# Optimization experiments

Hardware: AMD Instinct MI355X
Metric: run time of the kernel (lower is better)

## Reference

```python
import jax, jax.numpy as jnp
import numpy as np

B, D, T = 4, 1024, 512      # z: [B, input_dim, T]
V, CD = 32000, 4096          # codebook: [codebook_size, codebook_dim]
EPS = 1e-12                  # F.normalize default eps


def setup_inputs() -> dict:
    key = jax.random.key(0)
    k1, k2, k3, k4 = jax.random.split(key, 4)
    z = jax.random.normal(k1, (B, D, T), dtype=jnp.float32)
    codebook = jax.random.normal(k2, (V, CD), dtype=jnp.float32) * 0.02
    cb_w = jax.random.normal(k3, (D, CD), dtype=jnp.float32) * 0.02  # torch Linear weight [out,in]
    cb_b = jax.random.normal(k4, (D,), dtype=jnp.float32) * 0.02
    return {"z": z, "codebook": codebook, "cb_w": cb_w, "cb_b": cb_b}


def _l2norm(x):
    n = jnp.sqrt(jnp.sum(x * x, axis=1, keepdims=True))
    return x / jnp.maximum(n, EPS)


def reference(z, codebook, cb_w, cb_b):
    # stride == 1, use_cblinear == True -> z_e = z
    z_e = z                                              # [B, D, T]
    proj_cb = codebook @ cb_w.T + cb_b                    # [V, D] cb_proj(codebook)

    # decode_latents
    enc = jnp.transpose(z_e, (0, 2, 1)).reshape(-1, D)    # (B*T, D)
    enc_n = _l2norm(enc)
    cb_n = _l2norm(proj_cb)
    dist = (jnp.sum(enc_n * enc_n, axis=1, keepdims=True)
            - 2.0 * enc_n @ cb_n.T
            + jnp.sum(cb_n * cb_n, axis=1)[None, :])      # (B*T, V)
    indices = jnp.argmax(-dist, axis=1).reshape(B, T)     # argmin distance
    z_q = jnp.transpose(proj_cb[indices], (0, 2, 1))      # gather un-normalized codes -> [B, D, T]

    commitment_loss = jnp.mean((z_e - jax.lax.stop_gradient(z_q)) ** 2, axis=(1, 2))  # [B]
    codebook_loss = jnp.mean((z_q - jax.lax.stop_gradient(z_e)) ** 2, axis=(1, 2))    # [B]
    z_q_st = z_e + jax.lax.stop_gradient(z_q - z_e)       # straight-through
    return z_q_st, indices, commitment_loss, codebook_loss
```

## Files before the change

kernel.cpp:

```cpp
#include <hip/hip_runtime.h>
#include <hip/hip_bf16.h>
#include <math.h>

#define B_  4
#define D_  1024
#define T_  512
#define V_  32000
#define CD_ 4096
#define NR  (B_*T_)
#define VT2 (V_/256)

typedef __attribute__((ext_vector_type(8))) short short8v;
typedef __attribute__((ext_vector_type(4))) float f32x4;

#define MFMA16(a,b,c) __builtin_amdgcn_mfma_f32_16x16x32_bf16((a),(b),(c),0,0,0)

#define ASM_VMCNT8() asm volatile("s_waitcnt vmcnt(8)" ::: "memory")
#define ASM_VMCNT0() asm volatile("s_waitcnt vmcnt(0)" ::: "memory")
#define ASM_LGKM0()  asm volatile("s_waitcnt lgkmcnt(0)" ::: "memory")
#define SCHED_BAR()  __builtin_amdgcn_sched_barrier(0)

__device__ __forceinline__ unsigned short f2bf(float f) {
    return __builtin_bit_cast(unsigned short, __float2bfloat16(f));
}
__device__ __forceinline__ float bf2f(unsigned short u) {
    unsigned int v = ((unsigned int)u) << 16;
    return __builtin_bit_cast(float, v);
}
__device__ __forceinline__ void glds16(const unsigned short* g, unsigned short* l) {
    __builtin_amdgcn_global_load_lds(
        (const __attribute__((address_space(1))) unsigned int*)g,
        (__attribute__((address_space(3))) unsigned int*)l, 16, 0, 0);
}
__device__ __forceinline__ void gldsf(const float* g, float* l) {
    __builtin_amdgcn_global_load_lds(
        (const __attribute__((address_space(1))) unsigned int*)g,
        (__attribute__((address_space(3))) unsigned int*)l, 16, 0, 0);
}
__device__ __forceinline__ void cvt8(const float4& x, const float4& y,
                                     short8v& h, short8v& l) {
    float xs[8] = {x.x, x.y, x.z, x.w, y.x, y.y, y.z, y.w};
    #pragma unroll
    for (int e = 0; e < 8; ++e) {
        unsigned short hb = f2bf(xs[e]);
        h[e] = (short)hb;
        l[e] = (short)f2bf(xs[e] - bf2f(hb));
    }
}
__device__ __forceinline__ int xcd_swz(int wg, int nwg) {
    int q = nwg >> 3, r = nwg & 7;
    int x = wg & 7, o = wg >> 3;
    return (x < r ? x * (q + 1) : r * (q + 1) + (x - r) * q) + o;
}

__global__ __launch_bounds__(256) void vq_cvt(const float* __restrict__ x,
                                              unsigned short* __restrict__ hi,
                                              unsigned short* __restrict__ lo,
                                              size_t n4) {
    size_t stride = (size_t)gridDim.x * 256;
    for (size_t i = (size_t)blockIdx.x * 256 + threadIdx.x; i < n4; i += stride) {
        float4 v = *(const float4*)(x + 4 * i);
        float xs[4] = {v.x, v.y, v.z, v.w};
        ushort4 h, l;
        unsigned short* hp = (unsigned short*)&h;
        unsigned short* lp = (unsigned short*)&l;
        #pragma unroll
        for (int e = 0; e < 4; ++e) {
            hp[e] = f2bf(xs[e]);
            lp[e] = f2bf(xs[e] - bf2f(hp[e]));
        }
        *(ushort4*)(hi + 4 * i) = h;
        *(ushort4*)(lo + 4 * i) = l;
    }
}

__global__ __launch_bounds__(512, 2) void vq_gemm1_f(
    const float* __restrict__ Acb,
    const unsigned short* __restrict__ Bhp, const unsigned short* __restrict__ Blp,
    const float* __restrict__ bias,
    unsigned short* __restrict__ Phi, unsigned short* __restrict__ Plo)
{
    __shared__ float          Af[2][8192];
    __shared__ unsigned short Bh[2][8192];
    __shared__ unsigned short Bl[2][8192];
    const int wg = xcd_swz(blockIdx.x, (V_/256) * (D_/256));
    const int mt = (wg >> 2) * 256;
    const int nt = (wg & 3) * 256;
    const int lane = threadIdx.x & 63, w = threadIdx.x >> 6;
    const int wr = w >> 2, wc = w & 3;
    const int r16 = lane & 15, kg = lane >> 4;
    const int lane8 = lane * 8, wr8 = wr * 8, wc4 = wc * 4;

    f32x4 acc[8][4];
    #pragma unroll
    for (int i = 0; i < 8; ++i)
        #pragma unroll
        for (int j = 0; j < 4; ++j) acc[i][j] = (f32x4){0.f, 0.f, 0.f, 0.f};

#define STAGE1F(b, kk) do {                                                   \
    if (w < 4) {                                                              \
        _Pragma("unroll")                                                     \
        for (int j = 0; j < 4; ++j) {                                         \
            const int sub = w * 4 + j;                                        \
            const float* g0 = Acb + (size_t)(mt + sub*16 + r16) * CD_         \
                              + (kk) + kg * 4;                                \
            gldsf(g0,      &Af[b][sub*512]);                                  \
            gldsf(g0 + 16, &Af[b][sub*512 + 256]);                            \
        }                                                                     \
    } else if (w < 6) {                                                       \
        const int sb = (w - 4) * 8;                                           \
        _Pragma("unroll")                                                     \
        for (int j = 0; j < 8; ++j)                                           \
            glds16(Bhp + (size_t)(nt + (sb+j)*16 + r16) * CD_ + (kk) + kg*8,  \
                   &Bh[b][(sb+j)*512]);                                       \
    } else {                                                                  \
        const int sb = (w - 6) * 8;                                           \
        _Pragma("unroll")                                                     \
        for (int j = 0; j < 8; ++j)                                           \
            glds16(Blp + (size_t)(nt + (sb+j)*16 + r16) * CD_ + (kk) + kg*8,  \
                   &Bl[b][(sb+j)*512]);                                       \
    }                                                                         \
} while (0)

    STAGE1F(0, 0);
    ASM_VMCNT0();
    __builtin_amdgcn_s_barrier();
    SCHED_BAR();

    const int NT = CD_ / 32;
    const int afrag = (kg >> 1) * 256 + (kg & 1) * 128 + r16 * 4;
    for (int t = 0; t < NT; ++t) {
        const int cur = t & 1;
        if (t + 1 < NT) {
            STAGE1F(cur ^ 1, (size_t)(t + 1) * 32);
            ASM_VMCNT8();
        } else {
            ASM_VMCNT0();
        }
        __builtin_amdgcn_s_barrier();
        SCHED_BAR();
        short8v bh[4], bl[4];
        #pragma unroll
        for (int nf = 0; nf < 4; ++nf) {
            bh[nf] = *(const short8v*)&Bh[cur][(wc4 + nf) * 512 + lane8];
            bl[nf] = *(const short8v*)&Bl[cur][(wc4 + nf) * 512 + lane8];
        }
        #pragma unroll
        for (int g = 0; g < 4; ++g) {
            const float* f0 = &Af[cur][(wr8 + 2*g) * 512 + afrag];
            const float* f1 = &Af[cur][(wr8 + 2*g + 1) * 512 + afrag];
            float4 x0 = *(const float4*)f0, x1 = *(const float4*)(f0 + 64);
            float4 y0 = *(const float4*)f1, y1 = *(const float4*)(f1 + 64);
            short8v a0h, a0l, a1h, a1l;
            cvt8(x0, x1, a0h, a0l);
            cvt8(y0, y1, a1h, a1l);
            __builtin_amdgcn_s_setprio(1);
            #pragma unroll
            for (int nf = 0; nf < 4; ++nf) {
                acc[2*g][nf]   = MFMA16(a0h, bh[nf], acc[2*g][nf]);
                acc[2*g][nf]   = MFMA16(a0h, bl[nf], acc[2*g][nf]);
                acc[2*g][nf]   = MFMA16(a0l, bh[nf], acc[2*g][nf]);
                acc[2*g+1][nf] = MFMA16(a1h, bh[nf], acc[2*g+1][nf]);
                acc[2*g+1][nf] = MFMA16(a1h, bl[nf], acc[2*g+1][nf]);
                acc[2*g+1][nf] = MFMA16(a1l, bh[nf], acc[2*g+1][nf]);
            }
            __builtin_amdgcn_s_setprio(0);
        }
        ASM_LGKM0();
        __builtin_amdgcn_s_barrier();
        SCHED_BAR();
    }
#undef STAGE1F

    #pragma unroll
    for (int nf = 0; nf < 4; ++nf) {
        const int col = nt + wc * 64 + nf * 16 + r16;
        const float bv = bias[col];
        #pragma unroll
        for (int mf = 0; mf < 8; ++mf) {
            const int rbase = mt + wr * 128 + mf * 16 + kg * 4;
            #pragma unroll
            for (int r = 0; r < 4; ++r) {
                float vv = acc[mf][nf][r] + bv;
                unsigned short h = f2bf(vv);
                unsigned short l = f2bf(vv - bf2f(h));
                size_t o = (size_t)(rbase + r) * D_ + col;
                Phi[o] = h; Plo[o] = l;
            }
        }
    }
}

#define T8_PHASE(pp, EXTRA)                                                   \
    {                                                                         \
        short8v aAh = *(const short8v*)&smem[cur][0][(wr8 + 2*(pp)) * 512 + lane8];     \
        short8v aAl = *(const short8v*)&smem[cur][1][(wr8 + 2*(pp)) * 512 + lane8];     \
        short8v aBh = *(const short8v*)&smem[cur][0][(wr8 + 2*(pp) + 1) * 512 + lane8]; \
        short8v aBl = *(const short8v*)&smem[cur][1][(wr8 + 2*(pp) + 1) * 512 + lane8]; \
        EXTRA;                                                                \
        SCHED_BAR();                                                          \
        __builtin_amdgcn_s_barrier();                                         \
        ASM_LGKM0();                                                          \
        SCHED_BAR();                                                          \
        __builtin_amdgcn_s_setprio(1);                                        \
        _Pragma("unroll")                                                     \
        for (int nf = 0; nf < 4; ++nf) {                                      \
            acc[2*(pp)][nf]   = MFMA16(aAh, bh[nf], acc[2*(pp)][nf]);         \
            acc[2*(pp)][nf]   = MFMA16(aAh, bl[nf], acc[2*(pp)][nf]);         \
            acc[2*(pp)][nf]   = MFMA16(aAl, bh[nf], acc[2*(pp)][nf]);         \
            acc[2*(pp)+1][nf] = MFMA16(aBh, bh[nf], acc[2*(pp)+1][nf]);       \
            acc[2*(pp)+1][nf] = MFMA16(aBh, bl[nf], acc[2*(pp)+1][nf]);       \
            acc[2*(pp)+1][nf] = MFMA16(aBl, bh[nf], acc[2*(pp)+1][nf]);       \
        }                                                                     \
        __builtin_amdgcn_s_setprio(0);                                        \
        __builtin_amdgcn_s_barrier();                                         \
        SCHED_BAR();                                                          \
    }

__global__ __launch_bounds__(512, 2) void vq_gemm2_t8(
    const unsigned short* __restrict__ Ahp, const unsigned short* __restrict__ Alp,
    const unsigned short* __restrict__ Bhp, const unsigned short* __restrict__ Blp,
    const float* __restrict__ ninv,
    float* __restrict__ pmax, int* __restrict__ pidx)
{
    __shared__ unsigned short smem[2][4][8192];
    const int wg = xcd_swz(blockIdx.x, (NR/256) * VT2);
    const int nid = wg >> 3;
    const int mt = (wg & 7) * 256;
    const int nt = nid * 256;

    f32x4 acc[8][4];
    #pragma unroll
    for (int i = 0; i < 8; ++i)
        #pragma unroll
        for (int j = 0; j < 4; ++j) acc[i][j] = (f32x4){0.f, 0.f, 0.f, 0.f};
    const int lane = threadIdx.x & 63, w = threadIdx.x >> 6;
    const int wr = w >> 2, wc = w & 3;
    const int r16 = lane & 15, kg = lane >> 4;
    const int lane8 = lane * 8, wr8 = wr * 8, wc4 = wc * 4;
    const int pw = w >> 1;
    const unsigned short* gplane = (pw == 0) ? Ahp : (pw == 1) ? Alp
                                   : (pw == 2) ? Bhp : Blp;
    const int baseRow = (pw < 2 ? mt : nt) + (w & 1) * 128 + r16;
    const unsigned short* gsrc = gplane + (size_t)baseRow * D_ + kg * 8;
    unsigned short* lb0 = &smem[0][pw][(w & 1) * 4096 + lane8];
    unsigned short* lb1 = &smem[1][pw][(w & 1) * 4096 + lane8];
    #pragma unroll
    for (int q = 0; q < 8; ++q)
        glds16(gsrc + (size_t)q * 16 * D_, lb0 + q * 512);
    ASM_VMCNT0();
    __builtin_amdgcn_s_barrier();
    SCHED_BAR();
    const int NT = D_ / 32;
    for (int t = 0; t < NT; ++t) {
        const int cur = t & 1;
        unsigned short* lbN = cur ? lb0 : lb1;
        short8v bh[4], bl[4];
        #pragma unroll
        for (int nf = 0; nf < 4; ++nf) {
            bh[nf] = *(const short8v*)&smem[cur][2][(wc4 + nf) * 512 + lane8];
            bl[nf] = *(const short8v*)&smem[cur][3][(wc4 + nf) * 512 + lane8];
        }
        T8_PHASE(0,
            if (t + 1 < NT) {
                const size_t kof = (size_t)(t + 1) * 32;
                _Pragma("unroll")
                for (int q = 0; q < 8; ++q)
                    glds16(gsrc + kof + (size_t)q * 16 * D_, lbN + q * 512);
            })
        T8_PHASE(1, (void)0)
        T8_PHASE(2, (void)0)
        T8_PHASE(3, if (t + 1 < NT) { ASM_VMCNT0(); })
    }

    float* redv = (float*)&smem[0][0][0];
    int*   redi = (int*)&smem[0][0][2048];
    float nv[4];
    #pragma unroll
    for (int nf = 0; nf < 4; ++nf) nv[nf] = ninv[nt + wc * 64 + nf * 16 + r16];
    #pragma unroll
    for (int mf = 0; mf < 8; ++mf) {
        #pragma unroll
        for (int r = 0; r < 4; ++r) {
            float best = -INFINITY; int bi = 0x7fffffff;
            #pragma unroll
            for (int nf = 0; nf < 4; ++nf) {
                float v = acc[mf][nf][r] * nv[nf];
                int ci = nt + wc * 64 + nf * 16 + r16;
                if (v > best || (v == best && ci < bi)) { best = v; bi = ci; }
            }
            #pragma unroll
            for (int m = 8; m >= 1; m >>= 1) {
                float ov = __shfl_xor(best, m, 16);
                int   oi = __shfl_xor(bi,   m, 16);
                if (ov > best || (ov == best && oi < bi)) { best = ov; bi = oi; }
            }
            if (r16 == 0) {
                int rl = wr * 128 + mf * 16 + kg * 4 + r;
                redv[rl * 4 + wc] = best; redi[rl * 4 + wc] = bi;
            }
        }
    }
    __builtin_amdgcn_s_barrier();
    if (threadIdx.x < 256) {
        float best = -INFINITY; int bi = 0x7fffffff;
        #pragma unroll
        for (int c = 0; c < 4; ++c) {
            float v = redv[threadIdx.x * 4 + c];
            int   i = redi[threadIdx.x * 4 + c];
            if (v > best || (v == best && i < bi)) { best = v; bi = i; }
        }
        size_t o = (size_t)(mt + threadIdx.x) * VT2 + nid;
        pmax[o] = best; pidx[o] = bi;
    }
}

__global__ __launch_bounds__(256) void vq_norms_pl(const unsigned short* __restrict__ ph,
                                                   const unsigned short* __restrict__ pl,
                                                   float* __restrict__ ninv) {
    const int row  = blockIdx.x * 4 + (threadIdx.x >> 6);
    const int lane = threadIdx.x & 63;
    float s = 0.f;
    #pragma unroll
    for (int q = 0; q < 2; ++q) {
        size_t o = (size_t)row * D_ + q * 512 + lane * 8;
        short8v h = *(const short8v*)(ph + o);
        short8v l = *(const short8v*)(pl + o);
        #pragma unroll
        for (int e = 0; e < 8; ++e) {
            float x = bf2f((unsigned short)h[e]) + bf2f((unsigned short)l[e]);
            s += x * x;
        }
    }
    #pragma unroll
    for (int off = 32; off >= 1; off >>= 1) s += __shfl_down(s, off);
    if (lane == 0) ninv[row] = 1.0f / fmaxf(sqrtf(s), 1e-12f);
}

__global__ __launch_bounds__(256) void vq_transpose_cvt(const float* __restrict__ z,
                                                        unsigned short* __restrict__ ehi,
                                                        unsigned short* __restrict__ elo) {
    __shared__ float tile[64][65];
    const int b = blockIdx.z, t0 = blockIdx.x * 64, d0 = blockIdx.y * 64;
    const int lane = threadIdx.x & 63, sub = threadIdx.x >> 6;
    for (int dd = sub; dd < 64; dd += 4)
        tile[dd][lane] = z[((size_t)b * D_ + d0 + dd) * T_ + t0 + lane];
    __syncthreads();
    for (int tt = sub; tt < 64; tt += 4) {
        float v = tile[lane][tt];
        unsigned short h = f2bf(v);
        unsigned short l = f2bf(v - bf2f(h));
        size_t o = (size_t)(b * T_ + t0 + tt) * D_ + d0 + lane;
        ehi[o] = h; elo[o] = l;
    }
}

__global__ __launch_bounds__(256) void vq_argmerge(const float* __restrict__ pmax,
                                                   const int* __restrict__ pidx,
                                                   int* __restrict__ idxw,
                                                   float* __restrict__ outI,
                                                   int vt) {
    const int i = blockIdx.x * 256 + threadIdx.x;
    if (i >= NR) return;
    float best = -INFINITY; int bi = 0;
    for (int c = 0; c < vt; c++) {
        float v = pmax[(size_t)i * vt + c];
        int   ii = pidx[(size_t)i * vt + c];
        if (v > best || (v == best && ii < bi)) { best = v; bi = ii; }
    }
    idxw[i] = bi;
    outI[i] = (float)bi;
}

__global__ __launch_bounds__(256) void vq_gather_pl(const unsigned short* __restrict__ ph,
                                                    const unsigned short* __restrict__ pl,
                                                    const int* __restrict__ idxw,
                                                    const float* __restrict__ z,
                                                    float* __restrict__ out0,
                                                    float* __restrict__ lpart) {
    __shared__ float zq[64][65];
    __shared__ int idx_s[64];
    __shared__ float wsum[4];
    const int b = blockIdx.z, t0 = blockIdx.x * 64, d0 = blockIdx.y * 64;
    const int tid = threadIdx.x;
    const int lane = tid & 63, sub = tid >> 6;
    if (tid < 64) idx_s[tid] = idxw[b * T_ + t0 + tid];
    __syncthreads();
    for (int tt = sub; tt < 64; tt += 4) {
        size_t o = (size_t)idx_s[tt] * D_ + d0 + lane;
        zq[tt][lane] = bf2f(ph[o]) + bf2f(pl[o]);
    }
    __syncthreads();
    float lacc = 0.f;
    for (int dd = sub; dd < 64; dd += 4) {
        const size_t base = ((size_t)b * D_ + d0 + dd) * T_ + t0 + lane;
        float q = zq[lane][dd];
        float zv = z[base];
        out0[base] = q;
        float dv = zv - q;
        lacc += dv * dv;
    }
    #pragma unroll
    for (int off = 32; off >= 1; off >>= 1) lacc += __shfl_down(lacc, off);
    if (lane == 0) wsum[sub] = lacc;
    __syncthreads();
    if (tid == 0)
        lpart[(blockIdx.z * 16 + blockIdx.y) * 8 + blockIdx.x] =
            wsum[0] + wsum[1] + wsum[2] + wsum[3];
}

__global__ void vq_loss(const float* __restrict__ lpart, float* __restrict__ outL) {
    const int b = threadIdx.x;
    if (b >= B_) return;
    float s = 0.f;
    for (int q = 0; q < 128; q++) s += lpart[b * 128 + q];
    s /= (float)(D_ * T_);
    outL[b]      = s;
    outL[B_ + b] = s;
}

extern "C" void kernel_launch(void* const* d_in, const int* in_sizes, int n_in,
                              void* d_out, int out_size, void* d_ws, size_t ws_size,
                              hipStream_t stream) {
    const float* z        = (const float*)d_in[0];
    const float* codebook = (const float*)d_in[1];
    const float* cb_w     = (const float*)d_in[2];
    const float* cb_b     = (const float*)d_in[3];

    float* out0 = (float*)d_out;
    float* outI = out0 + (size_t)B_*D_*T_;
    float* outL = outI + NR;

    char* p = (char*)d_ws;
    auto alloc = [&](size_t bytes) { char* r = p; p += (bytes + 255) & ~(size_t)255; return r; };
    unsigned short* w_hi = (unsigned short*)alloc((size_t)D_ * CD_ * 2);
    unsigned short* w_lo = (unsigned short*)alloc((size_t)D_ * CD_ * 2);
    unsigned short* p_hi = (unsigned short*)alloc((size_t)V_ * D_ * 2);
    unsigned short* p_lo = (unsigned short*)alloc((size_t)V_ * D_ * 2);
    unsigned short* e_hi = (unsigned short*)alloc((size_t)NR * D_ * 2);
    unsigned short* e_lo = (unsigned short*)alloc((size_t)NR * D_ * 2);
    float* ninv  = (float*)alloc((size_t)V_ * 4);
    float* pmax  = (float*)alloc((size_t)NR * VT2 * 4);
    int*   pidx  = (int*)  alloc((size_t)NR * VT2 * 4);
    int*   idxw  = (int*)  alloc((size_t)NR * 4);
    float* lpart = (float*)alloc((size_t)2048 * 4);

    vq_cvt<<<512, 256, 0, stream>>>(cb_w, w_hi, w_lo, (size_t)D_ * CD_ / 4);
    vq_transpose_cvt<<<dim3(T_/64, D_/64, B_), 256, 0, stream>>>(z, e_hi, e_lo);

    vq_gemm1_f<<<(V_/256) * (D_/256), 512, 0, stream>>>(codebook, w_hi, w_lo,
                                                        cb_b, p_hi, p_lo);
    vq_norms_pl<<<V_/4, 256, 0, stream>>>(p_hi, p_lo, ninv);
    vq_gemm2_t8<<<(NR/256) * VT2, 512, 0, stream>>>(e_hi, e_lo, p_hi, p_lo,
                                                    ninv, pmax, pidx);
    vq_argmerge<<<NR/256, 256, 0, stream>>>(pmax, pidx, idxw, outI, VT2);
    vq_gather_pl<<<dim3(T_/64, D_/64, B_), 256, 0, stream>>>(p_hi, p_lo, idxw, z,
                                                             out0, lpart);
    vq_loss<<<1, 64, 0, stream>>>(lpart, outL);
}
```

Before: 1.573 ms.

## Pre-split codebook to bf16 planes and split-K the projection GEMM

Measured after the change: 1.733 ms. 10.1% more time.

```diff
diff --git a/kernel.cpp b/kernel.cpp
--- a/kernel.cpp
+++ b/kernel.cpp
@@ -9,6 +9,7 @@
 #define CD_ 4096
 #define NR  (B_*T_)
 #define VT2 (V_/256)
+#define NTILE1 ((V_/256)*(D_/256))
 
 typedef __attribute__((ext_vector_type(8))) short short8v;
 typedef __attribute__((ext_vector_type(4))) float f32x4;
@@ -28,11 +29,6 @@
     return __builtin_bit_cast(float, v);
 }
 __device__ __forceinline__ void glds16(const unsigned short* g, unsigned short* l) {
-    __builtin_amdgcn_global_load_lds(
-        (const __attribute__((address_space(1))) unsigned int*)g,
-        (__attribute__((address_space(3))) unsigned int*)l, 16, 0, 0);
-}
-__device__ __forceinline__ void gldsf(const float* g, float* l) {
     __builtin_amdgcn_global_load_lds(
         (const __attribute__((address_space(1))) unsigned int*)g,
         (__attribute__((address_space(3))) unsigned int*)l, 16, 0, 0);
@@ -74,22 +70,29 @@
     }
 }
 
-__global__ __launch_bounds__(512, 2) void vq_gemm1_f(
-    const float* __restrict__ Acb,
+__global__ __launch_bounds__(512, 2) void vq_gemm1_sk(
+    const unsigned short* __restrict__ Ahp, const unsigned short* __restrict__ Alp,
     const unsigned short* __restrict__ Bhp, const unsigned short* __restrict__ Blp,
-    const float* __restrict__ bias,
-    unsigned short* __restrict__ Phi, unsigned short* __restrict__ Plo)
+    float* __restrict__ pf, int nch)
 {
-    __shared__ float          Af[2][8192];
-    __shared__ unsigned short Bh[2][8192];
-    __shared__ unsigned short Bl[2][8192];
-    const int wg = xcd_swz(blockIdx.x, (V_/256) * (D_/256));
-    const int mt = (wg >> 2) * 256;
-    const int nt = (wg & 3) * 256;
+    __shared__ unsigned short smem[2][4][8192];
+    const int wg = xcd_swz(blockIdx.x, NTILE1 * nch);
+    const int kc = wg / NTILE1;
+    const int tl = wg - kc * NTILE1;
+    const int mt = (tl >> 2) * 256;
+    const int nt = (tl & 3) * 256;
+    const int kbase = kc * (CD_ / nch);
     const int lane = threadIdx.x & 63, w = threadIdx.x >> 6;
     const int wr = w >> 2, wc = w & 3;
     const int r16 = lane & 15, kg = lane >> 4;
     const int lane8 = lane * 8, wr8 = wr * 8, wc4 = wc * 4;
+    const int pw = w >> 1;
+    const unsigned short* gplane = (pw == 0) ? Ahp : (pw == 1) ? Alp
+                                   : (pw == 2) ? Bhp : Blp;
+    const int baseRow = (pw < 2 ? mt : nt) + (w & 1) * 128 + r16;
+    const unsigned short* gsrc = gplane + (size_t)baseRow * CD_ + kbase + kg * 8;
+    unsigned short* lb0 = &smem[0][pw][(w & 1) * 4096 + lane8];
+    unsigned short* lb1 = &smem[1][pw][(w & 1) * 4096 + lane8];
 
     f32x4 acc[8][4];
     #pragma unroll
@@ -97,42 +100,22 @@
         #pragma unroll
         for (int j = 0; j < 4; ++j) acc[i][j] = (f32x4){0.f, 0.f, 0.f, 0.f};
 
-#define STAGE1F(b, kk) do {                                                   \
-    if (w < 4) {                                                              \
-        _Pragma("unroll")                                                     \
-        for (int j = 0; j < 4; ++j) {                                         \
-            const int sub = w * 4 + j;                                        \
-            const float* g0 = Acb + (size_t)(mt + sub*16 + r16) * CD_         \
-                              + (kk) + kg * 4;                                \
-            gldsf(g0,      &Af[b][sub*512]);                                  \
-            gldsf(g0 + 16, &Af[b][sub*512 + 256]);                            \
-        }                                                                     \
-    } else if (w < 6) {                                                       \
-        const int sb = (w - 4) * 8;                                           \
-        _Pragma("unroll")                                                     \
-        for (int j = 0; j < 8; ++j)                                           \
-            glds16(Bhp + (size_t)(nt + (sb+j)*16 + r16) * CD_ + (kk) + kg*8,  \
-                   &Bh[b][(sb+j)*512]);                                       \
-    } else {                                                                  \
-        const int sb = (w - 6) * 8;                                           \
-        _Pragma("unroll")                                                     \
-        for (int j = 0; j < 8; ++j)                                           \
-            glds16(Blp + (size_t)(nt + (sb+j)*16 + r16) * CD_ + (kk) + kg*8,  \
-                   &Bl[b][(sb+j)*512]);                                       \
-    }                                                                         \
-} while (0)
-
-    STAGE1F(0, 0);
+    #pragma unroll
+    for (int q = 0; q < 8; ++q)
+        glds16(gsrc + (size_t)q * 16 * CD_, lb0 + q * 512);
     ASM_VMCNT0();
     __builtin_amdgcn_s_barrier();
     SCHED_BAR();
 
-    const int NT = CD_ / 32;
-    const int afrag = (kg >> 1) * 256 + (kg & 1) * 128 + r16 * 4;
+    const int NT = (CD_ / 32) / nch;
     for (int t = 0; t < NT; ++t) {
         const int cur = t & 1;
         if (t + 1 < NT) {
-            STAGE1F(cur ^ 1, (size_t)(t + 1) * 32);
+            unsigned short* lb = cur ? lb0 : lb1;
+            const size_t kof = (size_t)(t + 1) * 32;
+            #pragma unroll
+            for (int q = 0; q < 8; ++q)
+                glds16(gsrc + kof + (size_t)q * 16 * CD_, lb + q * 512);
             ASM_VMCNT8();
         } else {
             ASM_VMCNT0();
@@ -142,18 +125,15 @@
         short8v bh[4], bl[4];
         #pragma unroll
         for (int nf = 0; nf < 4; ++nf) {
-            bh[nf] = *(const short8v*)&Bh[cur][(wc4 + nf) * 512 + lane8];
-            bl[nf] = *(const short8v*)&Bl[cur][(wc4 + nf) * 512 + lane8];
+            bh[nf] = *(const short8v*)&smem[cur][2][(wc4 + nf) * 512 + lane8];
+            bl[nf] = *(const short8v*)&smem[cur][3][(wc4 + nf) * 512 + lane8];
         }
         #pragma unroll
         for (int g = 0; g < 4; ++g) {
-            const float* f0 = &Af[cur][(wr8 + 2*g) * 512 + afrag];
-            const float* f1 = &Af[cur][(wr8 + 2*g + 1) * 512 + afrag];
-            float4 x0 = *(const float4*)f0, x1 = *(const float4*)(f0 + 64);
-            float4 y0 = *(const float4*)f1, y1 = *(const float4*)(f1 + 64);
-            short8v a0h, a0l, a1h, a1l;
-            cvt8(x0, x1, a0h, a0l);
-            cvt8(y0, y1, a1h, a1l);
+            short8v a0h = *(const short8v*)&smem[cur][0][(wr8 + 2*g) * 512 + lane8];
+            short8v a0l = *(const short8v*)&smem[cur][1][(wr8 + 2*g) * 512 + lane8];
+            short8v a1h = *(const short8v*)&smem[cur][0][(wr8 + 2*g + 1) * 512 + lane8];
+            short8v a1l = *(const short8v*)&smem[cur][1][(wr8 + 2*g + 1) * 512 + lane8];
             __builtin_amdgcn_s_setprio(1);
             #pragma unroll
             for (int nf = 0; nf < 4; ++nf) {
@@ -170,7 +150,126 @@
         __builtin_amdgcn_s_barrier();
         SCHED_BAR();
     }
-#undef STAGE1F
+
+    float* out = pf + (size_t)kc * V_ * D_;
+    #pragma unroll
+    for (int nf = 0; nf < 4; ++nf) {
+        const int col = nt + wc * 64 + nf * 16 + r16;
+        #pragma unroll
+        for (int mf = 0; mf < 8; ++mf) {
+            const int rbase = mt + wr * 128 + mf * 16 + kg * 4;
+            #pragma unroll
+            for (int r = 0; r < 4; ++r)
+                out[(size_t)(rbase + r) * D_ + col] = acc[mf][nf][r];
+        }
+    }
+}
+
+__global__ __launch_bounds__(256) void vq_reduce(const float* __restrict__ pf, int nch,
+                                                 const float* __restrict__ bias,
+                                                 unsigned short* __restrict__ hi,
+                                                 unsigned short* __restrict__ lo) {
+    const size_t n4 = (size_t)V_ * D_ / 4;
+    size_t stride = (size_t)gridDim.x * 256;
+    for (size_t i = (size_t)blockIdx.x * 256 + threadIdx.x; i < n4; i += stride) {
+        float4 s = ((const float4*)pf)[i];
+        for (int c = 1; c < nch; ++c) {
+            float4 p = *(const float4*)(pf + (size_t)c * V_ * D_ + 4 * i);
+            s.x += p.x; s.y += p.y; s.z += p.z; s.w += p.w;
+        }
+        float4 b = ((const float4*)bias)[i & (D_/4 - 1)];
+        float xs[4] = {s.x + b.x, s.y + b.y, s.z + b.z, s.w + b.w};
+        ushort4 h, l;
+        unsigned short* hp = (unsigned short*)&h;
+        unsigned short* lp = (unsigned short*)&l;
+        #pragma unroll
+        for (int e = 0; e < 4; ++e) {
+            hp[e] = f2bf(xs[e]);
+            lp[e] = f2bf(xs[e] - bf2f(hp[e]));
+        }
+        *(ushort4*)(hi + 4 * i) = h;
+        *(ushort4*)(lo + 4 * i) = l;
+    }
+}
+
+__global__ __launch_bounds__(512, 2) void vq_gemm1_v2(
+    const unsigned short* __restrict__ Ahp, const unsigned short* __restrict__ Alp,
+    const unsigned short* __restrict__ Bhp, const unsigned short* __restrict__ Blp,
+    const float* __restrict__ bias,
+    unsigned short* __restrict__ Phi, unsigned short* __restrict__ Plo)
+{
+    __shared__ unsigned short smem[2][4][8192];
+    const int wg = xcd_swz(blockIdx.x, NTILE1);
+    const int mt = (wg >> 2) * 256;
+    const int nt = (wg & 3) * 256;
+    const int lane = threadIdx.x & 63, w = threadIdx.x >> 6;
+    const int wr = w >> 2, wc = w & 3;
+    const int r16 = lane & 15, kg = lane >> 4;
+    const int lane8 = lane * 8, wr8 = wr * 8, wc4 = wc * 4;
+    const int pw = w >> 1;
+    const unsigned short* gplane = (pw == 0) ? Ahp : (pw == 1) ? Alp
+                                   : (pw == 2) ? Bhp : Blp;
+    const int baseRow = (pw < 2 ? mt : nt) + (w & 1) * 128 + r16;
+    const unsigned short* gsrc = gplane + (size_t)baseRow * CD_ + kg * 8;
+    unsigned short* lb0 = &smem[0][pw][(w & 1) * 4096 + lane8];
+    unsigned short* lb1 = &smem[1][pw][(w & 1) * 4096 + lane8];
+
+    f32x4 acc[8][4];
+    #pragma unroll
+    for (int i = 0; i < 8; ++i)
+        #pragma unroll
+        for (int j = 0; j < 4; ++j) acc[i][j] = (f32x4){0.f, 0.f, 0.f, 0.f};
+
+    #pragma unroll
+    for (int q = 0; q < 8; ++q)
+        glds16(gsrc + (size_t)q * 16 * CD_, lb0 + q * 512);
+    ASM_VMCNT0();
+    __builtin_amdgcn_s_barrier();
+    SCHED_BAR();
+
+    const int NT = CD_ / 32;
+    for (int t = 0; t < NT; ++t) {
+        const int cur = t & 1;
+        if (t + 1 < NT) {
+            unsigned short* lb = cur ? lb0 : lb1;
+            const size_t kof = (size_t)(t + 1) * 32;
+            #pragma unroll
+            for (int q = 0; q < 8; ++q)
+                glds16(gsrc + kof + (size_t)q * 16 * CD_, lb + q * 512);
+            ASM_VMCNT8();
+        } else {
+            ASM_VMCNT0();
+        }
+        __builtin_amdgcn_s_barrier();
+        SCHED_BAR();
+        short8v bh[4], bl[4];
+        #pragma unroll
+        for (int nf = 0; nf < 4; ++nf) {
+            bh[nf] = *(const short8v*)&smem[cur][2][(wc4 + nf) * 512 + lane8];
+            bl[nf] = *(const short8v*)&smem[cur][3][(wc4 + nf) * 512 + lane8];
+        }
+        #pragma unroll
+        for (int g = 0; g < 4; ++g) {
+            short8v a0h = *(const short8v*)&smem[cur][0][(wr8 + 2*g) * 512 + lane8];
+            short8v a0l = *(const short8v*)&smem[cur][1][(wr8 + 2*g) * 512 + lane8];
+            short8v a1h = *(const short8v*)&smem[cur][0][(wr8 + 2*g + 1) * 512 + lane8];
+            short8v a1l = *(const short8v*)&smem[cur][1][(wr8 + 2*g + 1) * 512 + lane8];
+            __builtin_amdgcn_s_setprio(1);
+            #pragma unroll
+            for (int nf = 0; nf < 4; ++nf) {
+                acc[2*g][nf]   = MFMA16(a0h, bh[nf], acc[2*g][nf]);
+                acc[2*g][nf]   = MFMA16(a0h, bl[nf], acc[2*g][nf]);
+                acc[2*g][nf]   = MFMA16(a0l, bh[nf], acc[2*g][nf]);
+                acc[2*g+1][nf] = MFMA16(a1h, bh[nf], acc[2*g+1][nf]);
+                acc[2*g+1][nf] = MFMA16(a1h, bl[nf], acc[2*g+1][nf]);
+                acc[2*g+1][nf] = MFMA16(a1l, bh[nf], acc[2*g+1][nf]);
+            }
+            __builtin_amdgcn_s_setprio(0);
+        }
+        ASM_LGKM0();
+        __builtin_amdgcn_s_barrier();
+        SCHED_BAR();
+    }
 
     #pragma unroll
     for (int nf = 0; nf < 4; ++nf) {
@@ -213,7 +312,7 @@
             acc[2*(pp)+1][nf] = MFMA16(aBl, bh[nf], acc[2*(pp)+1][nf]);       \
         }                                                                     \
         __builtin_amdgcn_s_setprio(0);                                        \
-        __builtin_amdgcn_s_barrier();                                         \
+        __builtin_amdgcn_s_barrier();                                        \
         SCHED_BAR();                                                          \
     }
 
@@ -444,12 +543,28 @@
     int*   pidx  = (int*)  alloc((size_t)NR * VT2 * 4);
     int*   idxw  = (int*)  alloc((size_t)NR * 4);
     float* lpart = (float*)alloc((size_t)2048 * 4);
+    unsigned short* c_hi = (unsigned short*)alloc((size_t)V_ * CD_ * 2);
+    unsigned short* c_lo = (unsigned short*)alloc((size_t)V_ * CD_ * 2);
+    size_t need_v2 = (size_t)(p - (char*)d_ws);
+    float* pf = (float*)alloc((size_t)2 * V_ * D_ * 4);
+    size_t need_k2 = (size_t)(p - (char*)d_ws);
+    alloc((size_t)2 * V_ * D_ * 4);
+    size_t need_k4 = (size_t)(p - (char*)d_ws);
 
     vq_cvt<<<512, 256, 0, stream>>>(cb_w, w_hi, w_lo, (size_t)D_ * CD_ / 4);
     vq_transpose_cvt<<<dim3(T_/64, D_/64, B_), 256, 0, stream>>>(z, e_hi, e_lo);
-
-    vq_gemm1_f<<<(V_/256) * (D_/256), 512, 0, stream>>>(codebook, w_hi, w_lo,
-                                                        cb_b, p_hi, p_lo);
+    vq_cvt<<<4096, 256, 0, stream>>>(codebook, c_hi, c_lo, (size_t)V_ * CD_ / 4);
+
+    if (ws_size >= need_k4) {
+        vq_gemm1_sk<<<NTILE1 * 4, 512, 0, stream>>>(c_hi, c_lo, w_hi, w_lo, pf, 4);
+        vq_reduce<<<4096, 256, 0, stream>>>(pf, 4, cb_b, p_hi, p_lo);
+    } else if (ws_size >= need_k2) {
+        vq_gemm1_sk<<<NTILE1 * 2, 512, 0, stream>>>(c_hi, c_lo, w_hi, w_lo, pf, 2);
+        vq_reduce<<<4096, 256, 0, stream>>>(pf, 2, cb_b, p_hi, p_lo);
+    } else {
+        vq_gemm1_v2<<<NTILE1, 512, 0, stream>>>(c_hi, c_lo, w_hi, w_lo,
+                                                cb_b, p_hi, p_lo);
+    }
     vq_norms_pl<<<V_/4, 256, 0, stream>>>(p_hi, p_lo, ninv);
     vq_gemm2_t8<<<(NR/256) * VT2, 512, 0, stream>>>(e_hi, e_lo, p_hi, p_lo,
                                                     ninv, pmax, pidx);
```

## Use single-bf16 distance GEMM with top-k candidates and exact rescoring

Applied to the files above, without the earlier changes.

After: 2.546 ms. 61.8% more time.

```diff
diff --git a/kernel.cpp b/kernel.cpp
--- a/kernel.cpp
+++ b/kernel.cpp
@@ -9,6 +9,9 @@
 #define CD_ 4096
 #define NR  (B_*T_)
 #define VT2 (V_/256)
+#define NTILE1 ((V_/256)*(D_/256))
+#define NQ4 (VT2*4)
+#define NC8 8
 
 typedef __attribute__((ext_vector_type(8))) short short8v;
 typedef __attribute__((ext_vector_type(4))) float f32x4;
@@ -16,6 +19,7 @@
 #define MFMA16(a,b,c) __builtin_amdgcn_mfma_f32_16x16x32_bf16((a),(b),(c),0,0,0)
 
 #define ASM_VMCNT8() asm volatile("s_waitcnt vmcnt(8)" ::: "memory")
+#define ASM_VMCNT4() asm volatile("s_waitcnt vmcnt(4)" ::: "memory")
 #define ASM_VMCNT0() asm volatile("s_waitcnt vmcnt(0)" ::: "memory")
 #define ASM_LGKM0()  asm volatile("s_waitcnt lgkmcnt(0)" ::: "memory")
 #define SCHED_BAR()  __builtin_amdgcn_sched_barrier(0)
@@ -32,11 +36,6 @@
         (const __attribute__((address_space(1))) unsigned int*)g,
         (__attribute__((address_space(3))) unsigned int*)l, 16, 0, 0);
 }
-__device__ __forceinline__ void gldsf(const float* g, float* l) {
-    __builtin_amdgcn_global_load_lds(
-        (const __attribute__((address_space(1))) unsigned int*)g,
-        (__attribute__((address_space(3))) unsigned int*)l, 16, 0, 0);
-}
 __device__ __forceinline__ void cvt8(const float4& x, const float4& y,
                                      short8v& h, short8v& l) {
     float xs[8] = {x.x, x.y, x.z, x.w, y.x, y.y, y.z, y.w};
@@ -51,6 +50,11 @@
     int q = nwg >> 3, r = nwg & 7;
     int x = wg & 7, o = wg >> 3;
     return (x < r ? x * (q + 1) : r * (q + 1) + (x - r) * q) + o;
+}
+__device__ __forceinline__ void top2_ins(float& v1, int& i1, float& v2, int& i2,
+                                         float nv, int ni) {
+    if (nv > v1 || (nv == v1 && ni < i1)) { v2 = v1; i2 = i1; v1 = nv; i1 = ni; }
+    else if (nv > v2 || (nv == v2 && ni < i2)) { v2 = nv; i2 = ni; }
 }
 
 __global__ __launch_bounds__(256) void vq_cvt(const float* __restrict__ x,
@@ -71,123 +75,6 @@
         }
         *(ushort4*)(hi + 4 * i) = h;
         *(ushort4*)(lo + 4 * i) = l;
-    }
-}
-
-__global__ __launch_bounds__(512, 2) void vq_gemm1_f(
-    const float* __restrict__ Acb,
-    const unsigned short* __restrict__ Bhp, const unsigned short* __restrict__ Blp,
-    const float* __restrict__ bias,
-    unsigned short* __restrict__ Phi, unsigned short* __restrict__ Plo)
-{
-    __shared__ float          Af[2][8192];
-    __shared__ unsigned short Bh[2][8192];
-    __shared__ unsigned short Bl[2][8192];
-    const int wg = xcd_swz(blockIdx.x, (V_/256) * (D_/256));
-    const int mt = (wg >> 2) * 256;
-    const int nt = (wg & 3) * 256;
-    const int lane = threadIdx.x & 63, w = threadIdx.x >> 6;
-    const int wr = w >> 2, wc = w & 3;
-    const int r16 = lane & 15, kg = lane >> 4;
-    const int lane8 = lane * 8, wr8 = wr * 8, wc4 = wc * 4;
-
-    f32x4 acc[8][4];
-    #pragma unroll
-    for (int i = 0; i < 8; ++i)
-        #pragma unroll
-        for (int j = 0; j < 4; ++j) acc[i][j] = (f32x4){0.f, 0.f, 0.f, 0.f};
-
-#define STAGE1F(b, kk) do {                                                   \
-    if (w < 4) {                                                              \
-        _Pragma("unroll")                                                     \
-        for (int j = 0; j < 4; ++j) {                                         \
-            const int sub = w * 4 + j;                                        \
-            const float* g0 = Acb + (size_t)(mt + sub*16 + r16) * CD_         \
-                              + (kk) + kg * 4;                                \
-            gldsf(g0,      &Af[b][sub*512]);                                  \
-            gldsf(g0 + 16, &Af[b][sub*512 + 256]);                            \
-        }                                                                     \
-    } else if (w < 6) {                                                       \
-        const int sb = (w - 4) * 8;                                           \
-        _Pragma("unroll")                                                     \
-        for (int j = 0; j < 8; ++j)                                           \
-            glds16(Bhp + (size_t)(nt + (sb+j)*16 + r16) * CD_ + (kk) + kg*8,  \
-                   &Bh[b][(sb+j)*512]);                                       \
-    } else {                                                                  \
-        const int sb = (w - 6) * 8;                                           \
-        _Pragma("unroll")                                                     \
-        for (int j = 0; j < 8; ++j)                                           \
-            glds16(Blp + (size_t)(nt + (sb+j)*16 + r16) * CD_ + (kk) + kg*8,  \
-                   &Bl[b][(sb+j)*512]);                                       \
-    }                                                                         \
-} while (0)
-
-    STAGE1F(0, 0);
-    ASM_VMCNT0();
-    __builtin_amdgcn_s_barrier();
-    SCHED_BAR();
-
-    const int NT = CD_ / 32;
-    const int afrag = (kg >> 1) * 256 + (kg & 1) * 128 + r16 * 4;
-    for (int t = 0; t < NT; ++t) {
-        const int cur = t & 1;
-        if (t + 1 < NT) {
-            STAGE1F(cur ^ 1, (size_t)(t + 1) * 32);
-            ASM_VMCNT8();
-        } else {
-            ASM_VMCNT0();
-        }
-        __builtin_amdgcn_s_barrier();
-        SCHED_BAR();
-        short8v bh[4], bl[4];
-        #pragma unroll
-        for (int nf = 0; nf < 4; ++nf) {
-            bh[nf] = *(const short8v*)&Bh[cur][(wc4 + nf) * 512 + lane8];
-            bl[nf] = *(const short8v*)&Bl[cur][(wc4 + nf) * 512 + lane8];
-        }
-        #pragma unroll
-        for (int g = 0; g < 4; ++g) {
-            const float* f0 = &Af[cur][(wr8 + 2*g) * 512 + afrag];
-            const float* f1 = &Af[cur][(wr8 + 2*g + 1) * 512 + afrag];
-            float4 x0 = *(const float4*)f0, x1 = *(const float4*)(f0 + 64);
-            float4 y0 = *(const float4*)f1, y1 = *(const float4*)(f1 + 64);
-            short8v a0h, a0l, a1h, a1l;
-            cvt8(x0, x1, a0h, a0l);
-            cvt8(y0, y1, a1h, a1l);
-            __builtin_amdgcn_s_setprio(1);
-            #pragma unroll
-            for (int nf = 0; nf < 4; ++nf) {
-                acc[2*g][nf]   = MFMA16(a0h, bh[nf], acc[2*g][nf]);
-                acc[2*g][nf]   = MFMA16(a0h, bl[nf], acc[2*g][nf]);
-                acc[2*g][nf]   = MFMA16(a0l, bh[nf], acc[2*g][nf]);
-                acc[2*g+1][nf] = MFMA16(a1h, bh[nf], acc[2*g+1][nf]);
-                acc[2*g+1][nf] = MFMA16(a1h, bl[nf], acc[2*g+1][nf]);
-                acc[2*g+1][nf] = MFMA16(a1l, bh[nf], acc[2*g+1][nf]);
-            }
-            __builtin_amdgcn_s_setprio(0);
-        }
-        ASM_LGKM0();
-        __builtin_amdgcn_s_barrier();
-        SCHED_BAR();
-    }
-#undef STAGE1F
-
-    #pragma unroll
-    for (int nf = 0; nf < 4; ++nf) {
-        const int col = nt + wc * 64 + nf * 16 + r16;
-        const float bv = bias[col];
-        #pragma unroll
-        for (int mf = 0; mf < 8; ++mf) {
-            const int rbase = mt + wr * 128 + mf * 16 + kg * 4;
-            #pragma unroll
-            for (int r = 0; r < 4; ++r) {
-                float vv = acc[mf][nf][r] + bv;
-                unsigned short h = f2bf(vv);
-                unsigned short l = f2bf(vv - bf2f(h));
-                size_t o = (size_t)(rbase + r) * D_ + col;
-                Phi[o] = h; Plo[o] = l;
-            }
-        }
     }
 }
 
@@ -217,23 +104,16 @@
         SCHED_BAR();                                                          \
     }
 
-__global__ __launch_bounds__(512, 2) void vq_gemm2_t8(
+__global__ __launch_bounds__(512, 2) void vq_gemm1_t8(
     const unsigned short* __restrict__ Ahp, const unsigned short* __restrict__ Alp,
     const unsigned short* __restrict__ Bhp, const unsigned short* __restrict__ Blp,
-    const float* __restrict__ ninv,
-    float* __restrict__ pmax, int* __restrict__ pidx)
+    const float* __restrict__ bias,
+    unsigned short* __restrict__ Phi, unsigned short* __restrict__ Plo)
 {
     __shared__ unsigned short smem[2][4][8192];
-    const int wg = xcd_swz(blockIdx.x, (NR/256) * VT2);
-    const int nid = wg >> 3;
-    const int mt = (wg & 7) * 256;
-    const int nt = nid * 256;
-
-    f32x4 acc[8][4];
-    #pragma unroll
-    for (int i = 0; i < 8; ++i)
-        #pragma unroll
-        for (int j = 0; j < 4; ++j) acc[i][j] = (f32x4){0.f, 0.f, 0.f, 0.f};
+    const int wg = xcd_swz(blockIdx.x, NTILE1);
+    const int mt = (wg >> 2) * 256;
+    const int nt = (wg & 3) * 256;
     const int lane = threadIdx.x & 63, w = threadIdx.x >> 6;
     const int wr = w >> 2, wc = w & 3;
     const int r16 = lane & 15, kg = lane >> 4;
@@ -242,16 +122,23 @@
     const unsigned short* gplane = (pw == 0) ? Ahp : (pw == 1) ? Alp
                                    : (pw == 2) ? Bhp : Blp;
     const int baseRow = (pw < 2 ? mt : nt) + (w & 1) * 128 + r16;
-    const unsigned short* gsrc = gplane + (size_t)baseRow * D_ + kg * 8;
+    const unsigned short* gsrc = gplane + (size_t)baseRow * CD_ + kg * 8;
     unsigned short* lb0 = &smem[0][pw][(w & 1) * 4096 + lane8];
     unsigned short* lb1 = &smem[1][pw][(w & 1) * 4096 + lane8];
+
+    f32x4 acc[8][4];
+    #pragma unroll
+    for (int i = 0; i < 8; ++i)
+        #pragma unroll
+        for (int j = 0; j < 4; ++j) acc[i][j] = (f32x4){0.f, 0.f, 0.f, 0.f};
+
     #pragma unroll
     for (int q = 0; q < 8; ++q)
-        glds16(gsrc + (size_t)q * 16 * D_, lb0 + q * 512);
+        glds16(gsrc + (size_t)q * 16 * CD_, lb0 + q * 512);
     ASM_VMCNT0();
     __builtin_amdgcn_s_barrier();
     SCHED_BAR();
-    const int NT = D_ / 32;
+    const int NT = CD_ / 32;
     for (int t = 0; t < NT; ++t) {
         const int cur = t & 1;
         unsigned short* lbN = cur ? lb0 : lb1;
@@ -266,52 +153,204 @@
                 const size_t kof = (size_t)(t + 1) * 32;
                 _Pragma("unroll")
                 for (int q = 0; q < 8; ++q)
-                    glds16(gsrc + kof + (size_t)q * 16 * D_, lbN + q * 512);
+                    glds16(gsrc + kof + (size_t)q * 16 * CD_, lbN + q * 512);
             })
         T8_PHASE(1, (void)0)
         T8_PHASE(2, (void)0)
         T8_PHASE(3, if (t + 1 < NT) { ASM_VMCNT0(); })
     }
 
-    float* redv = (float*)&smem[0][0][0];
-    int*   redi = (int*)&smem[0][0][2048];
-    float nv[4];
-    #pragma unroll
-    for (int nf = 0; nf < 4; ++nf) nv[nf] = ninv[nt + wc * 64 + nf * 16 + r16];
-    #pragma unroll
-    for (int mf = 0; mf < 8; ++mf) {
-        #pragma unroll
-        for (int r = 0; r < 4; ++r) {
-            float best = -INFINITY; int bi = 0x7fffffff;
+    #pragma unroll
+    for (int nf = 0; nf < 4; ++nf) {
+        const int col = nt + wc * 64 + nf * 16 + r16;
+        const float bv = bias[col];
+        #pragma unroll
+        for (int mf = 0; mf < 8; ++mf) {
+            const int rbase = mt + wr * 128 + mf * 16 + kg * 4;
+            #pragma unroll
+            for (int r = 0; r < 4; ++r) {
+                float vv = acc[mf][nf][r] + bv;
+                unsigned short h = f2bf(vv);
+                unsigned short l = f2bf(vv - bf2f(h));
+                size_t o = (size_t)(rbase + r) * D_ + col;
+                Phi[o] = h; Plo[o] = l;
+            }
+        }
+    }
+}
+
+__global__ __launch_bounds__(512, 2) void vq_gemm2_c1(
+    const unsigned short* __restrict__ Eh, const unsigned short* __restrict__ Ph,
+    const float* __restrict__ ninv,
+    float* __restrict__ parrv, int* __restrict__ parri)
+{
+    __shared__ unsigned short smem[2][2][8192];
+    const int wg = xcd_swz(blockIdx.x, (NR/256) * VT2);
+    const int nid = wg >> 3;
+    const int mt = (wg & 7) * 256;
+    const int nt = nid * 256;
+    const int lane = threadIdx.x & 63, w = threadIdx.x >> 6;
+    const int wr = w >> 2, wc = w & 3;
+    const int r16 = lane & 15, kg = lane >> 4;
+    const int lane8 = lane * 8, wr8 = wr * 8, wc4 = wc * 4;
+    const int pw = w >> 2;
+    const int sq = (w & 3) * 4;
+    const unsigned short* gp = pw ? Ph : Eh;
+    const int baseRow = (pw ? nt : mt) + sq * 16 + r16;
+    const unsigned short* gsrc = gp + (size_t)baseRow * D_ + kg * 8;
+    unsigned short* lb0 = &smem[0][pw][sq * 512 + lane8];
+    unsigned short* lb1 = &smem[1][pw][sq * 512 + lane8];
+
+    f32x4 acc[8][4];
+    #pragma unroll
+    for (int i = 0; i < 8; ++i)
+        #pragma unroll
+        for (int j = 0; j < 4; ++j) acc[i][j] = (f32x4){0.f, 0.f, 0.f, 0.f};
+
+    #pragma unroll
+    for (int q = 0; q < 4; ++q)
+        glds16(gsrc + (size_t)q * 16 * D_, lb0 + q * 512);
+    ASM_VMCNT0();
+    __builtin_amdgcn_s_barrier();
+    SCHED_BAR();
+
+    const int NT = D_ / 32;
+    for (int t = 0; t < NT; ++t) {
+        const int cur = t & 1;
+        if (t + 1 < NT) {
+            unsigned short* lb = cur ? lb0 : lb1;
+            const size_t kof = (size_t)(t + 1) * 32;
+            #pragma unroll
+            for (int q = 0; q < 4; ++q)
+                glds16(gsrc + kof + (size_t)q * 16 * D_, lb + q * 512);
+            ASM_VMCNT4();
+        } else {
+            ASM_VMCNT0();
+        }
+        __builtin_amdgcn_s_barrier();
+        SCHED_BAR();
+        short8v bfr[4];
+        #pragma unroll
+        for (int nf = 0; nf < 4; ++nf)
+            bfr[nf] = *(const short8v*)&smem[cur][1][(wc4 + nf) * 512 + lane8];
+        #pragma unroll
+        for (int g = 0; g < 4; ++g) {
+            short8v a0 = *(const short8v*)&smem[cur][0][(wr8 + 2*g) * 512 + lane8];
+            short8v a1 = *(const short8v*)&smem[cur][0][(wr8 + 2*g + 1) * 512 + lane8];
+            __builtin_amdgcn_s_setprio(1);
             #pragma unroll
             for (int nf = 0; nf < 4; ++nf) {
-                float v = acc[mf][nf][r] * nv[nf];
+                acc[2*g][nf]   = MFMA16(a0, bfr[nf], acc[2*g][nf]);
+                acc[2*g+1][nf] = MFMA16(a1, bfr[nf], acc[2*g+1][nf]);
+            }
+            __builtin_amdgcn_s_setprio(0);
+        }
+        ASM_LGKM0();
+        __builtin_amdgcn_s_barrier();
+        SCHED_BAR();
+    }
+
+    const int qid = nid * 4 + wc;
+    float nv[4];
+    #pragma unroll
+    for (int nf = 0; nf < 4; ++nf) nv[nf] = ninv[nt + wc * 64 + nf * 16 + r16];
+    #pragma unroll
+    for (int mf = 0; mf < 8; ++mf) {
+        #pragma unroll
+        for (int r = 0; r < 4; ++r) {
+            float v1 = -INFINITY, v2 = -INFINITY;
+            int i1 = 0x7fffffff, i2 = 0x7fffffff;
+            #pragma unroll
+            for (int nf = 0; nf < 4; ++nf) {
+                float s = acc[mf][nf][r] * nv[nf];
                 int ci = nt + wc * 64 + nf * 16 + r16;
-                if (v > best || (v == best && ci < bi)) { best = v; bi = ci; }
+                top2_ins(v1, i1, v2, i2, s, ci);
             }
             #pragma unroll
             for (int m = 8; m >= 1; m >>= 1) {
-                float ov = __shfl_xor(best, m, 16);
-                int   oi = __shfl_xor(bi,   m, 16);
-                if (ov > best || (ov == best && oi < bi)) { best = ov; bi = oi; }
+                float ov1 = __shfl_xor(v1, m, 16); int oi1 = __shfl_xor(i1, m, 16);
+                float ov2 = __shfl_xor(v2, m, 16); int oi2 = __shfl_xor(i2, m, 16);
+                top2_ins(v1, i1, v2, i2, ov1, oi1);
+                top2_ins(v1, i1, v2, i2, ov2, oi2);
             }
             if (r16 == 0) {
-                int rl = wr * 128 + mf * 16 + kg * 4 + r;
-                redv[rl * 4 + wc] = best; redi[rl * 4 + wc] = bi;
+                const int row = mt + wr * 128 + mf * 16 + kg * 4 + r;
+                size_t off = (size_t)row * (NQ4 * 2) + qid * 2;
+                parrv[off] = v1;     parri[off] = i1;
+                parrv[off + 1] = v2; parri[off + 1] = i2;
             }
         }
     }
-    __builtin_amdgcn_s_barrier();
-    if (threadIdx.x < 256) {
-        float best = -INFINITY; int bi = 0x7fffffff;
-        #pragma unroll
-        for (int c = 0; c < 4; ++c) {
-            float v = redv[threadIdx.x * 4 + c];
-            int   i = redi[threadIdx.x * 4 + c];
-            if (v > best || (v == best && i < bi)) { best = v; bi = i; }
-        }
-        size_t o = (size_t)(mt + threadIdx.x) * VT2 + nid;
-        pmax[o] = best; pidx[o] = bi;
+}
+
+__global__ __launch_bounds__(256) void vq_top8(const float* __restrict__ parrv,
+                                               const int* __restrict__ parri,
+                                               int* __restrict__ cand) {
+    const int i = blockIdx.x * 256 + threadIdx.x;
+    if (i >= NR) return;
+    float v[NC8]; int id[NC8];
+    #pragma unroll
+    for (int k = 0; k < NC8; ++k) { v[k] = -INFINITY; id[k] = 0x7fffffff; }
+    const float* pv = parrv + (size_t)i * (NQ4 * 2);
+    const int*   pi = parri + (size_t)i * (NQ4 * 2);
+    for (int j = 0; j < NQ4 * 2; ++j) {
+        float nv = pv[j];
+        int   ni = pi[j];
+        #pragma unroll
+        for (int k = 0; k < NC8; ++k) {
+            bool better = (nv > v[k]) || (nv == v[k] && ni < id[k]);
+            float tv = v[k]; int ti = id[k];
+            if (better) { v[k] = nv; id[k] = ni; nv = tv; ni = ti; }
+        }
+    }
+    #pragma unroll
+    for (int k = 0; k < NC8; ++k) cand[i * NC8 + k] = id[k];
+}
+
+__global__ __launch_bounds__(256) void vq_rescore8(
+    const unsigned short* __restrict__ eh, const unsigned short* __restrict__ el,
+    const unsigned short* __restrict__ ph, const unsigned short* __restrict__ pl,
+    const float* __restrict__ ninv, const int* __restrict__ cand,
+    int* __restrict__ idxw, float* __restrict__ outI) {
+    __shared__ float e[D_];
+    __shared__ double wsum[NC8][4];
+    const int row = blockIdx.x;
+    const int tid = threadIdx.x, lane = tid & 63, wv = tid >> 6;
+    {
+        ushort4 h = *(const ushort4*)(eh + (size_t)row * D_ + tid * 4);
+        ushort4 l = *(const ushort4*)(el + (size_t)row * D_ + tid * 4);
+        const unsigned short* hp = (const unsigned short*)&h;
+        const unsigned short* lp = (const unsigned short*)&l;
+        #pragma unroll
+        for (int j = 0; j < 4; ++j)
+            e[tid * 4 + j] = bf2f(hp[j]) + bf2f(lp[j]);
+    }
+    __syncthreads();
+    for (int c = 0; c < NC8; ++c) {
+        int cv = cand[row * NC8 + c];
+        ushort4 h = *(const ushort4*)(ph + (size_t)cv * D_ + tid * 4);
+        ushort4 l = *(const ushort4*)(pl + (size_t)cv * D_ + tid * 4);
+        const unsigned short* hp = (const unsigned short*)&h;
+        const unsigned short* lp = (const unsigned short*)&l;
+        double s = 0.0;
+        #pragma unroll
+        for (int j = 0; j < 4; ++j)
+            s += (double)e[tid * 4 + j] * (double)(bf2f(hp[j]) + bf2f(lp[j]));
+        #pragma unroll
+        for (int off = 32; off >= 1; off >>= 1) s += __shfl_down(s, off);
+        if (lane == 0) wsum[c][wv] = s;
+    }
+    __syncthreads();
+    if (tid == 0) {
+        double best = -1.0e300; int bi = 0x7fffffff;
+        for (int c = 0; c < NC8; ++c) {
+            int cv = cand[row * NC8 + c];
+            double s = (wsum[c][0] + wsum[c][1] + wsum[c][2] + wsum[c][3])
+                       * (double)ninv[cv];
+            if (s > best || (s == best && cv < bi)) { best = s; bi = cv; }
+        }
+        idxw[row] = bi;
+        outI[row] = (float)bi;
     }
 }
 
@@ -353,23 +392,6 @@
         size_t o = (size_t)(b * T_ + t0 + tt) * D_ + d0 + lane;
         ehi[o] = h; elo[o] = l;
     }
-}
-
-__global__ __launch_bounds__(256) void vq_argmerge(const float* __restrict__ pmax,
-                                                   const int* __restrict__ pidx,
-                                                   int* __restrict__ idxw,
-                                                   float* __restrict__ outI,
-                                                   int vt) {
-    const int i = blockIdx.x * 256 + threadIdx.x;
-    if (i >= NR) return;
-    float best = -INFINITY; int bi = 0;
-    for (int c = 0; c < vt; c++) {
-        float v = pmax[(size_t)i * vt + c];
-        int   ii = pidx[(size_t)i * vt + c];
-        if (v > best || (v == best && ii < bi)) { best = v; bi = ii; }
-    }
-    idxw[i] = bi;
-    outI[i] = (float)bi;
 }
 
 __global__ __launch_bounds__(256) void vq_gather_pl(const unsigned short* __restrict__ ph,
@@ -440,20 +462,25 @@
     unsigned short* e_hi = (unsigned short*)alloc((size_t)NR * D_ * 2);
     unsigned short* e_lo = (unsigned short*)alloc((size_t)NR * D_ * 2);
     float* ninv  = (float*)alloc((size_t)V_ * 4);
-    float* pmax  = (float*)alloc((size_t)NR * VT2 * 4);
-    int*   pidx  = (int*)  alloc((size_t)NR * VT2 * 4);
+    float* parrv = (float*)alloc((size_t)NR * NQ4 * 2 * 4);
+    int*   parri = (int*)  alloc((size_t)NR * NQ4 * 2 * 4);
+    int*   cand  = (int*)  alloc((size_t)NR * NC8 * 4);
     int*   idxw  = (int*)  alloc((size_t)NR * 4);
     float* lpart = (float*)alloc((size_t)2048 * 4);
+    unsigned short* c_hi = (unsigned short*)alloc((size_t)V_ * CD_ * 2);
+    unsigned short* c_lo = (unsigned short*)alloc((size_t)V_ * CD_ * 2);
 
     vq_cvt<<<512, 256, 0, stream>>>(cb_w, w_hi, w_lo, (size_t)D_ * CD_ / 4);
     vq_transpose_cvt<<<dim3(T_/64, D_/64, B_), 256, 0, stream>>>(z, e_hi, e_lo);
-
-    vq_gemm1_f<<<(V_/256) * (D_/256), 512, 0, stream>>>(codebook, w_hi, w_lo,
-                                                        cb_b, p_hi, p_lo);
+    vq_cvt<<<4096, 256, 0, stream>>>(codebook, c_hi, c_lo, (size_t)V_ * CD_ / 4);
+
+    vq_gemm1_t8<<<NTILE1, 512, 0, stream>>>(c_hi, c_lo, w_hi, w_lo,
+                                            cb_b, p_hi, p_lo);
     vq_norms_pl<<<V_/4, 256, 0, stream>>>(p_hi, p_lo, ninv);
-    vq_gemm2_t8<<<(NR/256) * VT2, 512, 0, stream>>>(e_hi, e_lo, p_hi, p_lo,
-                                                    ninv, pmax, pidx);
-    vq_argmerge<<<NR/256, 256, 0, stream>>>(pmax, pidx, idxw, outI, VT2);
+    vq_gemm2_c1<<<(NR/256) * VT2, 512, 0, stream>>>(e_hi, p_hi, ninv, parrv, parri);
+    vq_top8<<<NR/256, 256, 0, stream>>>(parrv, parri, cand);
+    vq_rescore8<<<NR, 256, 0, stream>>>(e_hi, e_lo, p_hi, p_lo, ninv, cand,
+                                        idxw, outI);
     vq_gather_pl<<<dim3(T_/64, D_/64, B_), 256, 0, stream>>>(p_hi, p_lo, idxw, z,
                                                              out0, lpart);
     vq_loss<<<1, 64, 0, stream>>>(lpart, outL);
```
